# Optimization experiments

Measured on AMD Instinct MI355X. Metric: run time of the kernel, lower is better.

The kernel has to match this reference:

```python
import jax, jax.numpy as jnp
import numpy as np

B = 262144
STATE_DIM = 12
ACTION_DIM = 1
MSG_DIM = 32
MAX_CHILDREN = 2
EPS = 1e-12  # F.normalize default eps


def _l2norm(x):
    n = jnp.sqrt(jnp.sum(x * x, axis=-1, keepdims=True))
    return x / jnp.maximum(n, EPS)


def setup_inputs() -> dict:
    key = jax.random.key(0)
    ks = jax.random.split(key, 16)

    def lin(kw, kb, out_d, in_d):
        lim = 1.0 / np.sqrt(in_d)
        w = jax.random.uniform(kw, (out_d, in_d), jnp.float32, -lim, lim)
        b = jax.random.uniform(kb, (out_d,), jnp.float32, -lim, lim)
        return w, b

    state = jax.random.normal(ks[0], (B, STATE_DIM), jnp.float32)
    action = jax.random.normal(ks[1], (B, ACTION_DIM), jnp.float32)

    # ModelUp (sNet): fc1, fc2, fc3
    up_w1, up_b1 = lin(ks[2], ks[3], 64, STATE_DIM + ACTION_DIM)
    up_w2, up_b2 = lin(ks[4], ks[5], 64, 64 + MSG_DIM * MAX_CHILDREN)
    up_w3, up_b3 = lin(ks[6], ks[7], MSG_DIM, 64)

    # ModelDownAction.model = MLPBase(msg_dim + action_dim + msg_dim, msg_dim)
    dyn_w1, dyn_b1 = lin(ks[8], ks[9], 400, MSG_DIM + ACTION_DIM + MSG_DIM)
    dyn_w2, dyn_b2 = lin(ks[10], ks[11], 300, 400)
    dyn_w3, dyn_b3 = lin(ks[12], ks[13], MSG_DIM, 300)

    return dict(state=state, action=action,
                up_w1=up_w1, up_b1=up_b1, up_w2=up_w2, up_b2=up_b2,
                up_w3=up_w3, up_b3=up_b3,
                dyn_w1=dyn_w1, dyn_b1=dyn_b1, dyn_w2=dyn_w2, dyn_b2=dyn_b2,
                dyn_w3=dyn_w3, dyn_b3=dyn_b3)


def reference(state, action,
              up_w1, up_b1, up_w2, up_b2, up_w3, up_b3,
              dyn_w1, dyn_b1, dyn_w2, dyn_b2, dyn_w3, dyn_b3):
    # num_limbs == 1, parents = [-1], td = bu = True, disable_fold = True
    x = state                              # (B, state_dim)
    u = action                             # (B, 1)

    # ---- bottom_up_transmission(0): ModelUp with all-zero child messages ----
    m_children = jnp.zeros((B, MSG_DIM * MAX_CHILDREN), x.dtype)
    xu = jnp.concatenate([x, u], axis=-1)
    xu = _l2norm(xu @ up_w1.T + up_b1)                       # (B, 64)
    xum = jnp.tanh(jnp.concatenate([xu, m_children], axis=-1))
    xum = jnp.tanh(xum @ up_w2.T + up_b2)                    # (B, 64)
    msg_up = _l2norm(xum @ up_w3.T + up_b3)                  # (B, msg_dim)

    # ---- top_down_transmission(0): ModelDownAction, state := msg_up ----
    # parent_msg = zeros, self_children_idx = 0 -> msg_in = zeros slice
    msg_in = jnp.zeros((B, MSG_DIM), x.dtype)
    xum2 = jnp.concatenate([msg_up, u, msg_in], axis=-1)     # (B, 2*msg_dim+1)
    h = jax.nn.relu(xum2 @ dyn_w1.T + dyn_b1)                # (B, 400)
    h = jax.nn.relu(h @ dyn_w2.T + dyn_b2)                   # (B, 300)
    delta = h @ dyn_w3.T + dyn_b3                            # (B, msg_dim)

    # stack over num_limbs=1 then squeeze -> (B, msg_dim)
    return delta
```

## Files before the change

### kernel.cpp

```cpp
#include <hip/hip_runtime.h>
#include <stdint.h>

typedef short s16x8 __attribute__((ext_vector_type(8)));
typedef float f32x16 __attribute__((ext_vector_type(16)));
typedef unsigned int u32;
typedef unsigned int u32x2 __attribute__((ext_vector_type(2)));

#define NFRAG 336
#define WS_USHORTS (NFRAG*512)
#define PANEL_FRAGS 14
#define PANEL_BYTES (PANEL_FRAGS*1024)
#define LDS_BYTES (3*PANEL_BYTES)

#define MFMA(a,b,c) __builtin_amdgcn_mfma_f32_32x32x16_bf16((a),(b),(c),0,0,0)

__device__ __forceinline__ unsigned short f2bf(float f){
  u32 x = __builtin_bit_cast(u32, f);
  x += 0x7fffu + ((x >> 16) & 1u);
  return (unsigned short)(x >> 16);
}

__device__ __forceinline__ float bfhi(float b){
  return __builtin_bit_cast(float, (u32)f2bf(b) << 16);
}

__device__ __forceinline__ u32 pkbf(float a, float b){
  u32 r;
  asm("v_cvt_pk_bf16_f32 %0, %1, %2" : "=v"(r) : "v"(a), "v"(b));
  return r;
}

__device__ __forceinline__ float fast_tanh(float x){
  float ax = fabsf(x);
  float e = __expf(-2.0f * ax);
  float r = (1.0f - e) * __builtin_amdgcn_rcpf(1.0f + e);
  return x < 0.0f ? -r : r;
}

__device__ __forceinline__ float halfsum(float s){
  return s + __shfl_xor(s, 32);
}

__device__ __forceinline__ void tile2frags(const f32x16 v, s16x8& f0, s16x8& f1){
  u32 w00 = pkbf(v[0],  v[1]),  w01 = pkbf(v[2],  v[3]);
  u32 w10 = pkbf(v[4],  v[5]),  w11 = pkbf(v[6],  v[7]);
  u32 w20 = pkbf(v[8],  v[9]),  w21 = pkbf(v[10], v[11]);
  u32 w30 = pkbf(v[12], v[13]), w31 = pkbf(v[14], v[15]);
  u32x2 p0 = __builtin_amdgcn_permlane32_swap(w00, w10, false, false);
  u32x2 p1 = __builtin_amdgcn_permlane32_swap(w01, w11, false, false);
  u32x2 p2 = __builtin_amdgcn_permlane32_swap(w20, w30, false, false);
  u32x2 p3 = __builtin_amdgcn_permlane32_swap(w21, w31, false, false);
  int4 r0, r1;
  r0.x = (int)p0[0]; r0.y = (int)p1[0]; r0.z = (int)p0[1]; r0.w = (int)p1[1];
  r1.x = (int)p2[0]; r1.y = (int)p3[0]; r1.z = (int)p2[1]; r1.w = (int)p3[1];
  f0 = __builtin_bit_cast(s16x8, r0);
  f1 = __builtin_bit_cast(s16x8, r1);
}

__global__ void wconv_kernel(const float* __restrict__ uw1, const float* __restrict__ ub1,
                             const float* __restrict__ uw2, const float* __restrict__ ub2,
                             const float* __restrict__ uw3, const float* __restrict__ ub3,
                             const float* __restrict__ dw1, const float* __restrict__ db1,
                             const float* __restrict__ dw2, const float* __restrict__ db2,
                             const float* __restrict__ dw3, const float* __restrict__ db3,
                             unsigned short* __restrict__ wp)
{
  int i = blockIdx.x*256 + threadIdx.x;
  if (i >= WS_USHORTS) return;
  int f    = i >> 9;
  int lane = (i >> 3) & 63;
  int j    = i & 7;
  int row  = lane & 31;
  int k8   = (lane >> 5)*8 + j;
  float v = 0.0f;
  if (f < 2){
    int feat = f*32 + row; int k = k8;
    if (k < 13) v = uw1[feat*13 + k];
    else if (k == 13) v = ub1[feat];
    else if (k == 14) v = ub1[feat] - bfhi(ub1[feat]);
  } else if (f < 12){
    int t = f - 2; int kt = t >> 1, nt = t & 1;
    int feat = nt*32 + row; int k = kt*16 + k8;
    if (k < 64) v = uw2[feat*128 + k];
    else if (k == 64) v = ub2[feat];
    else if (k == 65) v = ub2[feat] - bfhi(ub2[feat]);
  } else if (f < 17){
    int kt = f - 12; int feat = row; int k = kt*16 + k8;
    if (k < 64) v = uw3[feat*64 + k];
    else if (k == 64) v = ub3[feat];
    else if (k == 65) v = ub3[feat] - bfhi(ub3[feat]);
  } else if (f < 56){
    int t = f - 17; int nt = t/3, kt = t%3;
    int feat = nt*32 + row; int k = kt*16 + k8;
    if (feat < 400){
      if (k < 33) v = dw1[feat*65 + k];
      else if (k == 33) v = db1[feat];
      else if (k == 34) v = db1[feat] - bfhi(db1[feat]);
    } else if ((feat == 400 || feat == 401) && k == 33) v = 1.0f;
  } else {
    int t = f - 56; int n = t/56; int r = t%56;
    if (r < 52){
      int kf = r >> 1, nt = r & 1;
      int feat = n*64 + nt*32 + row; int k = kf*16 + k8;
      if (feat < 300){
        if (k < 400) v = dw2[feat*400 + k];
        else if (k == 400) v = db2[feat];
        else if (k == 401) v = db2[feat] - bfhi(db2[feat]);
      } else if ((feat == 300 || feat == 301) && k == 400) v = 1.0f;
    } else {
      int kt = n*4 + (r - 52); int feat = row; int k = kt*16 + k8;
      if (k < 300) v = dw3[feat*300 + k];
      else if (k == 300) v = db3[feat];
      else if (k == 301) v = db3[feat] - bfhi(db3[feat]);
    }
  }
  wp[i] = f2bf(v);
}

__device__ __forceinline__ s16x8 fragF(const char* sm, int f, int ln){
  return *(const s16x8*)(sm + ((f/PANEL_FRAGS) % 3)*PANEL_BYTES
                            + (f % PANEL_FRAGS)*1024 + ln*16);
}

__device__ __forceinline__ void stage14(const unsigned short* wp, char* sm, int panel, int tid){
  char* dst = sm + (panel % 3)*PANEL_BYTES;
  const char* src = (const char*)wp + (size_t)panel*PANEL_BYTES;
  #pragma unroll
  for (int j = 0; j < 3; ++j){
    int off = j*4096 + tid*16;
    __builtin_amdgcn_global_load_lds(
      (const __attribute__((address_space(1))) unsigned int*)(src + off),
      (__attribute__((address_space(3))) unsigned int*)(dst + off), 16, 0, 0);
  }
  int off3 = 12288 + (tid & 127)*16;
  __builtin_amdgcn_global_load_lds(
    (const __attribute__((address_space(1))) unsigned int*)(src + off3),
    (__attribute__((address_space(3))) unsigned int*)(dst + off3), 16, 0, 0);
}

#define BND(P) { \
  __syncthreads(); \
  if ((P)+2 <= 23) stage14(wp, sm, (P)+2, tid); \
}

#define TAIL1(aSrc, oA, oB) { \
  _Pragma("unroll") \
  for (int r = 0; r < 16; ++r) aSrc[r] = fmaxf(aSrc[r], 0.f); \
  tile2frags(aSrc, oA, oB); }

#define D1MM(f0_, acc) { \
  __builtin_amdgcn_s_setprio(1); \
  acc = MFMA(fragF(sm, (f0_)+0, ln), mf0, acc); \
  acc = MFMA(fragF(sm, (f0_)+1, ln), mf1, acc); \
  acc = MFMA(fragF(sm, (f0_)+2, ln), mf2, acc); \
  __builtin_amdgcn_s_setprio(0); }

#define D2R(fb, r0, r1, A0, A1) { \
  __builtin_amdgcn_s_setprio(1); \
  _Pragma("unroll") \
  for (int r = (r0); r < (r1); ++r){ \
    s16x8 hb = h1f[r>>1]; \
    if (r & 1) A1 = MFMA(fragF(sm, (fb)+r, ln), hb, A1); \
    else       A0 = MFMA(fragF(sm, (fb)+r, ln), hb, A0); \
  } \
  __builtin_amdgcn_s_setprio(0); }

#define LOADD3W(fb) { \
  d3w0 = fragF(sm, (fb)+52, ln); \
  d3w1 = fragF(sm, (fb)+53, ln); \
  d3w2 = fragF(sm, (fb)+54, ln); \
  d3w3 = fragF(sm, (fb)+55, ln); }

#define TAILD2_RELU(A0, A1) { \
  _Pragma("unroll") \
  for (int r = 0; r < 16; ++r){ \
    A0[r] = fmaxf(A0[r], 0.f); \
    A1[r] = fmaxf(A1[r], 0.f); \
  } }
#define TAILD2_CVT(A0, A1) { \
  tile2frags(A0, cT0, cT1); \
  tile2frags(A1, cT2, cT3); }
#define TAILD2_D3() { \
  __builtin_amdgcn_s_setprio(1); \
  acc3 = MFMA(d3w0, cT0, acc3); \
  acc3 = MFMA(d3w1, cT1, acc3); \
  acc3 = MFMA(d3w2, cT2, acc3); \
  acc3 = MFMA(d3w3, cT3, acc3); \
  __builtin_amdgcn_s_setprio(0); }

#define CHUNKN(fb, P0, C0_, C1_, PR0, PR1) { \
  BND(P0) \
  C0_ = vzero; C1_ = vzero; \
  D2R(fb, 0, 14, C0_, C1_) \
  TAILD2_RELU(PR0, PR1) \
  BND((P0)+1) \
  D2R(fb, 14, 28, C0_, C1_) \
  TAILD2_CVT(PR0, PR1) \
  BND((P0)+2) \
  D2R(fb, 28, 42, C0_, C1_) \
  TAILD2_D3() \
  BND((P0)+3) \
  D2R(fb, 42, 52, C0_, C1_) \
  LOADD3W(fb) \
}

__global__ __launch_bounds__(256, 2) void fused_kernel(
    const float* __restrict__ state, const float* __restrict__ action,
    const unsigned short* __restrict__ wp, float* __restrict__ out)
{
  __shared__ __align__(1024) char sm[LDS_BYTES];

  const int tid = threadIdx.x;
  const int ln  = tid & 63;
  const int wid = tid >> 6;
  const int c   = ln & 31;
  const int h   = ln >> 5;
  const int rowb = blockIdx.x*128 + wid*32;

  const f32x16 vzero = {};

  const float* xr = state + (size_t)(rowb + c)*12;
  float u = action[rowb + c];
  float4 xa, xbr;
  if (h == 0){
    xa  = *(const float4*)xr;
    xbr = *(const float4*)(xr + 4);
  } else {
    xa  = *(const float4*)(xr + 8);
  }

  stage14(wp, sm, 0, tid);
  stage14(wp, sm, 1, tid);
  BND(0)

  float4 xb = (h == 0) ? xbr : float4{u, 1.0f, 1.0f, 0.0f};
  int4 xw;
  xw.x = pkbf(xa.x, xa.y); xw.y = pkbf(xa.z, xa.w);
  xw.z = pkbf(xb.x, xb.y); xw.w = pkbf(xb.z, xb.w);
  s16x8 xfrag = __builtin_bit_cast(s16x8, xw);
  int4 ow = {0,0,0,0}; if (h == 0) ow.x = 0x3F803F80;
  s16x8 onef = __builtin_bit_cast(s16x8, ow);
  int4 mw = {0,0,0,0};
  if (h == 0){ mw.x = pkbf(u, 1.0f); mw.y = 0x3F80; }
  s16x8 mf2 = __builtin_bit_cast(s16x8, mw);

  s16x8 mf0, mf1;
  {
    s16x8 xf0, xf1, xf2, xf3, tf0, tf1, tf2, tf3;
    {
      f32x16 a0 = {}, a1 = {};
      a0 = MFMA(fragF(sm, 0, ln), xfrag, a0);
      a1 = MFMA(fragF(sm, 1, ln), xfrag, a1);
      float s = 0.f;
      #pragma unroll
      for (int r = 0; r < 16; ++r) s += a0[r]*a0[r] + a1[r]*a1[r];
      s = halfsum(s);
      float inv = __builtin_amdgcn_rsqf(fmaxf(s, 1e-24f));
      #pragma unroll
      for (int r = 0; r < 16; ++r){
        a0[r] = fast_tanh(a0[r]*inv);
        a1[r] = fast_tanh(a1[r]*inv);
      }
      tile2frags(a0, xf0, xf1);
      tile2frags(a1, xf2, xf3);
    }
    {
      f32x16 a0 = {}, a1 = {};
      __builtin_amdgcn_s_setprio(1);
      a0 = MFMA(fragF(sm, 2, ln), xf0, a0);  a1 = MFMA(fragF(sm, 3, ln), xf0, a1);
      a0 = MFMA(fragF(sm, 4, ln), xf1, a0);  a1 = MFMA(fragF(sm, 5, ln), xf1, a1);
      a0 = MFMA(fragF(sm, 6, ln), xf2, a0);  a1 = MFMA(fragF(sm, 7, ln), xf2, a1);
      a0 = MFMA(fragF(sm, 8, ln), xf3, a0);  a1 = MFMA(fragF(sm, 9, ln), xf3, a1);
      a0 = MFMA(fragF(sm,10, ln), onef, a0); a1 = MFMA(fragF(sm,11, ln), onef, a1);
      __builtin_amdgcn_s_setprio(0);
      #pragma unroll
      for (int r = 0; r < 16; ++r){
        a0[r] = fast_tanh(a0[r]);
        a1[r] = fast_tanh(a1[r]);
      }
      tile2frags(a0, tf0, tf1);
      tile2frags(a1, tf2, tf3);
    }
    {
      f32x16 m = {};
      __builtin_amdgcn_s_setprio(1);
      m = MFMA(fragF(sm,12, ln), tf0, m);
      m = MFMA(fragF(sm,13, ln), tf1, m);
      __builtin_amdgcn_s_setprio(0);
      BND(1)
      __builtin_amdgcn_s_setprio(1);
      m = MFMA(fragF(sm,14, ln), tf2, m);
      m = MFMA(fragF(sm,15, ln), tf3, m);
      m = MFMA(fragF(sm,16, ln), onef, m);
      __builtin_amdgcn_s_setprio(0);
      float s = 0.f;
      #pragma unroll
      for (int r = 0; r < 16; ++r) s += m[r]*m[r];
      s = halfsum(s);
      float inv = __builtin_amdgcn_rsqf(fmaxf(s, 1e-24f));
      #pragma unroll
      for (int r = 0; r < 16; ++r) m[r] *= inv;
      tile2frags(m, mf0, mf1);
    }
  }

  s16x8 h1f[26];
  f32x16 aX = vzero, aY = vzero;
  D1MM(17, aX)
  D1MM(20, aY)  TAIL1(aX, h1f[0],  h1f[1])
  aX = vzero; D1MM(23, aX)  TAIL1(aY, h1f[2],  h1f[3])
  aY = vzero;
  __builtin_amdgcn_s_setprio(1);
  aY = MFMA(fragF(sm, 26, ln), mf0, aY);
  aY = MFMA(fragF(sm, 27, ln), mf1, aY);
  __builtin_amdgcn_s_setprio(0);
  BND(2)
  __builtin_amdgcn_s_setprio(1);
  aY = MFMA(fragF(sm, 28, ln), mf2, aY);
  __builtin_amdgcn_s_setprio(0);
  TAIL1(aX, h1f[4], h1f[5])
  aX = vzero; D1MM(29, aX)  TAIL1(aY, h1f[6],  h1f[7])
  aY = vzero; D1MM(32, aY)  TAIL1(aX, h1f[8],  h1f[9])
  aX = vzero; D1MM(35, aX)  TAIL1(aY, h1f[10], h1f[11])
  aY = vzero; D1MM(38, aY)  TAIL1(aX, h1f[12], h1f[13])
  aX = vzero;
  __builtin_amdgcn_s_setprio(1);
  aX = MFMA(fragF(sm, 41, ln), mf0, aX);
  __builtin_amdgcn_s_setprio(0);
  BND(3)
  __builtin_amdgcn_s_setprio(1);
  aX = MFMA(fragF(sm, 42, ln), mf1, aX);
  aX = MFMA(fragF(sm, 43, ln), mf2, aX);
  __builtin_amdgcn_s_setprio(0);
  TAIL1(aY, h1f[14], h1f[15])
  aY = vzero; D1MM(44, aY)  TAIL1(aX, h1f[16], h1f[17])
  aX = vzero; D1MM(47, aX)  TAIL1(aY, h1f[18], h1f[19])
  aY = vzero; D1MM(50, aY)  TAIL1(aX, h1f[20], h1f[21])
  aX = vzero; D1MM(53, aX)  TAIL1(aY, h1f[22], h1f[23])

  f32x16 acc3 = vzero;
  f32x16 dA0, dA1, dB0, dB1;
  s16x8 d3w0, d3w1, d3w2, d3w3, cT0, cT1, cT2, cT3;

  {
    BND(4)
    dA0 = vzero; dA1 = vzero;
    D2R(56, 0, 14, dA0, dA1)
    TAIL1(aX, h1f[24], h1f[25])
    BND(5)
    D2R(56, 14, 28, dA0, dA1)
    BND(6)
    D2R(56, 28, 42, dA0, dA1)
    BND(7)
    D2R(56, 42, 52, dA0, dA1)
    LOADD3W(56)
  }
  CHUNKN(112,  8, dB0, dB1, dA0, dA1)
  CHUNKN(168, 12, dA0, dA1, dB0, dB1)
  CHUNKN(224, 16, dB0, dB1, dA0, dA1)
  CHUNKN(280, 20, dA0, dA1, dB0, dB1)
  TAILD2_RELU(dA0, dA1)
  TAILD2_CVT(dA0, dA1)
  TAILD2_D3()

  float* op = out + (size_t)(rowb + c)*32;
  #pragma unroll
  for (int p = 0; p < 4; ++p){
    float4 v4 = {acc3[4*p+0], acc3[4*p+1], acc3[4*p+2], acc3[4*p+3]};
    *(float4*)(op + p*8 + h*4) = v4;
  }
}

extern "C" void kernel_launch(void* const* d_in, const int* in_sizes, int n_in,
                              void* d_out, int out_size, void* d_ws, size_t ws_size,
                              hipStream_t stream)
{
  const float* state  = (const float*)d_in[0];
  const float* action = (const float*)d_in[1];
  const float* up_w1  = (const float*)d_in[2];
  const float* up_b1  = (const float*)d_in[3];
  const float* up_w2  = (const float*)d_in[4];
  const float* up_b2  = (const float*)d_in[5];
  const float* up_w3  = (const float*)d_in[6];
  const float* up_b3  = (const float*)d_in[7];
  const float* dyn_w1 = (const float*)d_in[8];
  const float* dyn_b1 = (const float*)d_in[9];
  const float* dyn_w2 = (const float*)d_in[10];
  const float* dyn_b2 = (const float*)d_in[11];
  const float* dyn_w3 = (const float*)d_in[12];
  const float* dyn_b3 = (const float*)d_in[13];
  unsigned short* wp = (unsigned short*)d_ws;

  hipLaunchKernelGGL(wconv_kernel, dim3((WS_USHORTS + 255)/256), dim3(256), 0, stream,
                     up_w1, up_b1, up_w2, up_b2, up_w3, up_b3,
                     dyn_w1, dyn_b1, dyn_w2, dyn_b2, dyn_w3, dyn_b3, wp);
  hipLaunchKernelGGL(fused_kernel, dim3(262144/128), dim3(256), 0, stream,
                     state, action, wp, (float*)d_out);
}
```

Before: 92.42 us.

## Load odd dyn-layer-2 weight fragments straight from global into registers

Half of the layer-2 weight fragments (the odd ones) are now read directly from global memory into registers a stage ahead, instead of through LDS. The remaining fragments still come through the LDS panels. Barriers are replaced with an explicit partial vmcnt wait plus s_barrier, so the direct global loads can stay in flight across barriers. This aims to halve the LDS read traffic in the dominant layer, at the cost of more VGPRs for prefetched fragments, fragile hand-counted vmcnt values, and redundant global or L2 reads per wave.

```diff
diff --git a/kernel.cpp b/kernel.cpp
--- a/kernel.cpp
+++ b/kernel.cpp
@@ -122,6 +122,10 @@
                             + (f % PANEL_FRAGS)*1024 + ln*16);
 }
 
+__device__ __forceinline__ s16x8 fragG(const unsigned short* wp, int f, int ln){
+  return *(const s16x8*)(wp + (size_t)f*512 + ln*8);
+}
+
 __device__ __forceinline__ void stage14(const unsigned short* wp, char* sm, int panel, int tid){
   char* dst = sm + (panel % 3)*PANEL_BYTES;
   const char* src = (const char*)wp + (size_t)panel*PANEL_BYTES;
@@ -138,9 +142,30 @@
     (__attribute__((address_space(3))) unsigned int*)(dst + off3), 16, 0, 0);
 }
 
-#define BND(P) { \
-  __syncthreads(); \
+#define STR_(x) #x
+#define STR(x) STR_(x)
+#define BNDW(P, W) { \
+  asm volatile("s_waitcnt vmcnt(" STR(W) ") lgkmcnt(0)" ::: "memory"); \
+  __builtin_amdgcn_s_barrier(); \
+  __builtin_amdgcn_sched_barrier(0); \
   if ((P)+2 <= 23) stage14(wp, sm, (P)+2, tid); \
+}
+
+#define ISSUE7(fb, base, B) { \
+  B##0 = fragG(wp, (fb)+(base)+1,  ln); \
+  B##1 = fragG(wp, (fb)+(base)+3,  ln); \
+  B##2 = fragG(wp, (fb)+(base)+5,  ln); \
+  B##3 = fragG(wp, (fb)+(base)+7,  ln); \
+  B##4 = fragG(wp, (fb)+(base)+9,  ln); \
+  B##5 = fragG(wp, (fb)+(base)+11, ln); \
+  B##6 = fragG(wp, (fb)+(base)+13, ln); \
+}
+#define ISSUE5(fb, B) { \
+  B##0 = fragG(wp, (fb)+43, ln); \
+  B##1 = fragG(wp, (fb)+45, ln); \
+  B##2 = fragG(wp, (fb)+47, ln); \
+  B##3 = fragG(wp, (fb)+49, ln); \
+  B##4 = fragG(wp, (fb)+51, ln); \
 }
 
 #define TAIL1(aSrc, oA, oB) { \
@@ -155,14 +180,36 @@
   acc = MFMA(fragF(sm, (f0_)+2, ln), mf2, acc); \
   __builtin_amdgcn_s_setprio(0); }
 
-#define D2R(fb, r0, r1, A0, A1) { \
+#define D2RX14(fb, base, B, A0, A1) { \
   __builtin_amdgcn_s_setprio(1); \
-  _Pragma("unroll") \
-  for (int r = (r0); r < (r1); ++r){ \
-    s16x8 hb = h1f[r>>1]; \
-    if (r & 1) A1 = MFMA(fragF(sm, (fb)+r, ln), hb, A1); \
-    else       A0 = MFMA(fragF(sm, (fb)+r, ln), hb, A0); \
-  } \
+  A0 = MFMA(fragF(sm,(fb)+(base)+0, ln), h1f[((base)+0)>>1],  A0); \
+  A1 = MFMA(B##0,                        h1f[((base)+1)>>1],  A1); \
+  A0 = MFMA(fragF(sm,(fb)+(base)+2, ln), h1f[((base)+2)>>1],  A0); \
+  A1 = MFMA(B##1,                        h1f[((base)+3)>>1],  A1); \
+  A0 = MFMA(fragF(sm,(fb)+(base)+4, ln), h1f[((base)+4)>>1],  A0); \
+  A1 = MFMA(B##2,                        h1f[((base)+5)>>1],  A1); \
+  A0 = MFMA(fragF(sm,(fb)+(base)+6, ln), h1f[((base)+6)>>1],  A0); \
+  A1 = MFMA(B##3,                        h1f[((base)+7)>>1],  A1); \
+  A0 = MFMA(fragF(sm,(fb)+(base)+8, ln), h1f[((base)+8)>>1],  A0); \
+  A1 = MFMA(B##4,                        h1f[((base)+9)>>1],  A1); \
+  A0 = MFMA(fragF(sm,(fb)+(base)+10,ln), h1f[((base)+10)>>1], A0); \
+  A1 = MFMA(B##5,                        h1f[((base)+11)>>1], A1); \
+  A0 = MFMA(fragF(sm,(fb)+(base)+12,ln), h1f[((base)+12)>>1], A0); \
+  A1 = MFMA(B##6,                        h1f[((base)+13)>>1], A1); \
+  __builtin_amdgcn_s_setprio(0); }
+
+#define D2RX10(fb, B, A0, A1) { \
+  __builtin_amdgcn_s_setprio(1); \
+  A0 = MFMA(fragF(sm,(fb)+42, ln), h1f[21], A0); \
+  A1 = MFMA(B##0,                  h1f[21], A1); \
+  A0 = MFMA(fragF(sm,(fb)+44, ln), h1f[22], A0); \
+  A1 = MFMA(B##1,                  h1f[22], A1); \
+  A0 = MFMA(fragF(sm,(fb)+46, ln), h1f[23], A0); \
+  A1 = MFMA(B##2,                  h1f[23], A1); \
+  A0 = MFMA(fragF(sm,(fb)+48, ln), h1f[24], A0); \
+  A1 = MFMA(B##3,                  h1f[24], A1); \
+  A0 = MFMA(fragF(sm,(fb)+50, ln), h1f[25], A0); \
+  A1 = MFMA(B##4,                  h1f[25], A1); \
   __builtin_amdgcn_s_setprio(0); }
 
 #define LOADD3W(fb) { \
@@ -188,19 +235,23 @@
   acc3 = MFMA(d3w3, cT3, acc3); \
   __builtin_amdgcn_s_setprio(0); }
 
-#define CHUNKN(fb, P0, C0_, C1_, PR0, PR1) { \
-  BND(P0) \
+#define CHUNKX(fb, P0, C0_, C1_, PR0, PR1, ISSUE_NEXT, WLAST) { \
+  BNDW(P0, 11) \
+  ISSUE7(fb, 14, gB) \
   C0_ = vzero; C1_ = vzero; \
-  D2R(fb, 0, 14, C0_, C1_) \
+  D2RX14(fb, 0, gA, C0_, C1_) \
   TAILD2_RELU(PR0, PR1) \
-  BND((P0)+1) \
-  D2R(fb, 14, 28, C0_, C1_) \
+  BNDW((P0)+1, 11) \
+  ISSUE7(fb, 28, gA) \
+  D2RX14(fb, 14, gB, C0_, C1_) \
   TAILD2_CVT(PR0, PR1) \
-  BND((P0)+2) \
-  D2R(fb, 28, 42, C0_, C1_) \
+  BNDW((P0)+2, 11) \
+  ISSUE5(fb, gB) \
+  D2RX14(fb, 28, gA, C0_, C1_) \
   TAILD2_D3() \
-  BND((P0)+3) \
-  D2R(fb, 42, 52, C0_, C1_) \
+  BNDW((P0)+3, WLAST) \
+  ISSUE_NEXT \
+  D2RX10(fb, gB, C0_, C1_) \
   LOADD3W(fb) \
 }
 
@@ -218,6 +269,8 @@
   const int rowb = blockIdx.x*128 + wid*32;
 
   const f32x16 vzero = {};
+  s16x8 gA0, gA1, gA2, gA3, gA4, gA5, gA6;
+  s16x8 gB0, gB1, gB2, gB3, gB4, gB5, gB6;
 
   const float* xr = state + (size_t)(rowb + c)*12;
   float u = action[rowb + c];
@@ -231,7 +284,7 @@
 
   stage14(wp, sm, 0, tid);
   stage14(wp, sm, 1, tid);
-  BND(0)
+  BNDW(0, 4)
 
   float4 xb = (h == 0) ? xbr : float4{u, 1.0f, 1.0f, 0.0f};
   int4 xw;
@@ -287,7 +340,7 @@
       m = MFMA(fragF(sm,12, ln), tf0, m);
       m = MFMA(fragF(sm,13, ln), tf1, m);
       __builtin_amdgcn_s_setprio(0);
-      BND(1)
+      BNDW(1, 4)
       __builtin_amdgcn_s_setprio(1);
       m = MFMA(fragF(sm,14, ln), tf2, m);
       m = MFMA(fragF(sm,15, ln), tf3, m);
@@ -314,7 +367,7 @@
   aY = MFMA(fragF(sm, 26, ln), mf0, aY);
   aY = MFMA(fragF(sm, 27, ln), mf1, aY);
   __builtin_amdgcn_s_setprio(0);
-  BND(2)
+  BNDW(2, 4)
   __builtin_amdgcn_s_setprio(1);
   aY = MFMA(fragF(sm, 28, ln), mf2, aY);
   __builtin_amdgcn_s_setprio(0);
@@ -327,7 +380,8 @@
   __builtin_amdgcn_s_setprio(1);
   aX = MFMA(fragF(sm, 41, ln), mf0, aX);
   __builtin_amdgcn_s_setprio(0);
-  BND(3)
+  BNDW(3, 4)
+  ISSUE7(56, 0, gA)
   __builtin_amdgcn_s_setprio(1);
   aX = MFMA(fragF(sm, 42, ln), mf1, aX);
   aX = MFMA(fragF(sm, 43, ln), mf2, aX);
@@ -343,22 +397,26 @@
   s16x8 d3w0, d3w1, d3w2, d3w3, cT0, cT1, cT2, cT3;
 
   {
-    BND(4)
+    BNDW(4, 11)
+    ISSUE7(56, 14, gB)
     dA0 = vzero; dA1 = vzero;
-    D2R(56, 0, 14, dA0, dA1)
+    D2RX14(56, 0, gA, dA0, dA1)
     TAIL1(aX, h1f[24], h1f[25])
-    BND(5)
-    D2R(56, 14, 28, dA0, dA1)
-    BND(6)
-    D2R(56, 28, 42, dA0, dA1)
-    BND(7)
-    D2R(56, 42, 52, dA0, dA1)
+    BNDW(5, 11)
+    ISSUE7(56, 28, gA)
+    D2RX14(56, 14, gB, dA0, dA1)
+    BNDW(6, 11)
+    ISSUE5(56, gB)
+    D2RX14(56, 28, gA, dA0, dA1)
+    BNDW(7, 9)
+    ISSUE7(112, 0, gA)
+    D2RX10(56, gB, dA0, dA1)
     LOADD3W(56)
   }
-  CHUNKN(112,  8, dB0, dB1, dA0, dA1)
-  CHUNKN(168, 12, dA0, dA1, dB0, dB1)
-  CHUNKN(224, 16, dB0, dB1, dA0, dA1)
-  CHUNKN(280, 20, dA0, dA1, dB0, dB1)
+  CHUNKX(112,  8, dB0, dB1, dA0, dA1, ISSUE7(168, 0, gA), 9)
+  CHUNKX(168, 12, dA0, dA1, dB0, dB1, ISSUE7(224, 0, gA), 9)
+  CHUNKX(224, 16, dB0, dB1, dA0, dA1, ISSUE7(280, 0, gA), 9)
+  CHUNKX(280, 20, dA0, dA1, dB0, dB1, , 5)
   TAILD2_RELU(dA0, dA1)
   TAILD2_CVT(dA0, dA1)
   TAILD2_D3()
```

New measurement: 163.9 us. 77.3% more time.

## Shrink LDS weight panels to 8 fragments and raise occupancy to 4 blocks

Applied to the files above, without the earlier changes.

Cuts each triple-buffered LDS weight panel from 14 to 8 fragments, shrinking shared memory per block from 42KB to 24KB. It raises launch bounds to 4 blocks per CU and reschedules every panel boundary barrier across all layers to match the finer panels. The aim is more resident waves to hide latency, at the cost of more barriers and a tighter per-thread register budget. That budget may force spills of the 26 hidden fragments and the accumulators.

```diff
diff --git a/kernel.cpp b/kernel.cpp
--- a/kernel.cpp
+++ b/kernel.cpp
@@ -8,7 +8,7 @@
 
 #define NFRAG 336
 #define WS_USHORTS (NFRAG*512)
-#define PANEL_FRAGS 14
+#define PANEL_FRAGS 8
 #define PANEL_BYTES (PANEL_FRAGS*1024)
 #define LDS_BYTES (3*PANEL_BYTES)
 
@@ -122,25 +122,21 @@
                             + (f % PANEL_FRAGS)*1024 + ln*16);
 }
 
-__device__ __forceinline__ void stage14(const unsigned short* wp, char* sm, int panel, int tid){
+__device__ __forceinline__ void stage8(const unsigned short* wp, char* sm, int panel, int tid){
   char* dst = sm + (panel % 3)*PANEL_BYTES;
   const char* src = (const char*)wp + (size_t)panel*PANEL_BYTES;
   #pragma unroll
-  for (int j = 0; j < 3; ++j){
+  for (int j = 0; j < 2; ++j){
     int off = j*4096 + tid*16;
     __builtin_amdgcn_global_load_lds(
       (const __attribute__((address_space(1))) unsigned int*)(src + off),
       (__attribute__((address_space(3))) unsigned int*)(dst + off), 16, 0, 0);
   }
-  int off3 = 12288 + (tid & 127)*16;
-  __builtin_amdgcn_global_load_lds(
-    (const __attribute__((address_space(1))) unsigned int*)(src + off3),
-    (__attribute__((address_space(3))) unsigned int*)(dst + off3), 16, 0, 0);
 }
 
 #define BND(P) { \
   __syncthreads(); \
-  if ((P)+2 <= 23) stage14(wp, sm, (P)+2, tid); \
+  if ((P)+2 <= 41) stage8(wp, sm, (P)+2, tid); \
 }
 
 #define TAIL1(aSrc, oA, oB) { \
@@ -188,23 +184,29 @@
   acc3 = MFMA(d3w3, cT3, acc3); \
   __builtin_amdgcn_s_setprio(0); }
 
-#define CHUNKN(fb, P0, C0_, C1_, PR0, PR1) { \
+#define CHUNKP(fb, P0, C0_, C1_, PR0, PR1) { \
   BND(P0) \
   C0_ = vzero; C1_ = vzero; \
-  D2R(fb, 0, 14, C0_, C1_) \
+  D2R(fb, 0, 8, C0_, C1_) \
   TAILD2_RELU(PR0, PR1) \
   BND((P0)+1) \
-  D2R(fb, 14, 28, C0_, C1_) \
+  D2R(fb, 8, 16, C0_, C1_) \
   TAILD2_CVT(PR0, PR1) \
   BND((P0)+2) \
-  D2R(fb, 28, 42, C0_, C1_) \
+  D2R(fb, 16, 24, C0_, C1_) \
   TAILD2_D3() \
   BND((P0)+3) \
-  D2R(fb, 42, 52, C0_, C1_) \
+  D2R(fb, 24, 32, C0_, C1_) \
+  BND((P0)+4) \
+  D2R(fb, 32, 40, C0_, C1_) \
+  BND((P0)+5) \
+  D2R(fb, 40, 48, C0_, C1_) \
+  BND((P0)+6) \
+  D2R(fb, 48, 52, C0_, C1_) \
   LOADD3W(fb) \
 }
 
-__global__ __launch_bounds__(256, 2) void fused_kernel(
+__global__ __launch_bounds__(256, 4) void fused_kernel(
     const float* __restrict__ state, const float* __restrict__ action,
     const unsigned short* __restrict__ wp, float* __restrict__ out)
 {
@@ -229,8 +231,8 @@
     xa  = *(const float4*)(xr + 8);
   }
 
-  stage14(wp, sm, 0, tid);
-  stage14(wp, sm, 1, tid);
+  stage8(wp, sm, 0, tid);
+  stage8(wp, sm, 1, tid);
   BND(0)
 
   float4 xb = (h == 0) ? xbr : float4{u, 1.0f, 1.0f, 0.0f};
@@ -270,6 +272,9 @@
       a0 = MFMA(fragF(sm, 2, ln), xf0, a0);  a1 = MFMA(fragF(sm, 3, ln), xf0, a1);
       a0 = MFMA(fragF(sm, 4, ln), xf1, a0);  a1 = MFMA(fragF(sm, 5, ln), xf1, a1);
       a0 = MFMA(fragF(sm, 6, ln), xf2, a0);  a1 = MFMA(fragF(sm, 7, ln), xf2, a1);
+      __builtin_amdgcn_s_setprio(0);
+      BND(1)
+      __builtin_amdgcn_s_setprio(1);
       a0 = MFMA(fragF(sm, 8, ln), xf3, a0);  a1 = MFMA(fragF(sm, 9, ln), xf3, a1);
       a0 = MFMA(fragF(sm,10, ln), onef, a0); a1 = MFMA(fragF(sm,11, ln), onef, a1);
       __builtin_amdgcn_s_setprio(0);
@@ -286,11 +291,11 @@
       __builtin_amdgcn_s_setprio(1);
       m = MFMA(fragF(sm,12, ln), tf0, m);
       m = MFMA(fragF(sm,13, ln), tf1, m);
-      __builtin_amdgcn_s_setprio(0);
-      BND(1)
-      __builtin_amdgcn_s_setprio(1);
       m = MFMA(fragF(sm,14, ln), tf2, m);
       m = MFMA(fragF(sm,15, ln), tf3, m);
+      __builtin_amdgcn_s_setprio(0);
+      BND(2)
+      __builtin_amdgcn_s_setprio(1);
       m = MFMA(fragF(sm,16, ln), onef, m);
       __builtin_amdgcn_s_setprio(0);
       float s = 0.f;
@@ -308,33 +313,43 @@
   f32x16 aX = vzero, aY = vzero;
   D1MM(17, aX)
   D1MM(20, aY)  TAIL1(aX, h1f[0],  h1f[1])
-  aX = vzero; D1MM(23, aX)  TAIL1(aY, h1f[2],  h1f[3])
-  aY = vzero;
-  __builtin_amdgcn_s_setprio(1);
-  aY = MFMA(fragF(sm, 26, ln), mf0, aY);
-  aY = MFMA(fragF(sm, 27, ln), mf1, aY);
-  __builtin_amdgcn_s_setprio(0);
-  BND(2)
-  __builtin_amdgcn_s_setprio(1);
-  aY = MFMA(fragF(sm, 28, ln), mf2, aY);
-  __builtin_amdgcn_s_setprio(0);
-  TAIL1(aX, h1f[4], h1f[5])
+  aX = vzero;
+  __builtin_amdgcn_s_setprio(1);
+  aX = MFMA(fragF(sm, 23, ln), mf0, aX);
+  __builtin_amdgcn_s_setprio(0);
+  BND(3)
+  __builtin_amdgcn_s_setprio(1);
+  aX = MFMA(fragF(sm, 24, ln), mf1, aX);
+  aX = MFMA(fragF(sm, 25, ln), mf2, aX);
+  __builtin_amdgcn_s_setprio(0);
+  TAIL1(aY, h1f[2], h1f[3])
+  aY = vzero; D1MM(26, aY)  TAIL1(aX, h1f[4],  h1f[5])
   aX = vzero; D1MM(29, aX)  TAIL1(aY, h1f[6],  h1f[7])
+  BND(4)
   aY = vzero; D1MM(32, aY)  TAIL1(aX, h1f[8],  h1f[9])
   aX = vzero; D1MM(35, aX)  TAIL1(aY, h1f[10], h1f[11])
-  aY = vzero; D1MM(38, aY)  TAIL1(aX, h1f[12], h1f[13])
+  aY = vzero;
+  __builtin_amdgcn_s_setprio(1);
+  aY = MFMA(fragF(sm, 38, ln), mf0, aY);
+  aY = MFMA(fragF(sm, 39, ln), mf1, aY);
+  __builtin_amdgcn_s_setprio(0);
+  BND(5)
+  __builtin_amdgcn_s_setprio(1);
+  aY = MFMA(fragF(sm, 40, ln), mf2, aY);
+  __builtin_amdgcn_s_setprio(0);
+  TAIL1(aX, h1f[12], h1f[13])
+  aX = vzero; D1MM(41, aX)  TAIL1(aY, h1f[14], h1f[15])
+  aY = vzero; D1MM(44, aY)  TAIL1(aX, h1f[16], h1f[17])
   aX = vzero;
   __builtin_amdgcn_s_setprio(1);
-  aX = MFMA(fragF(sm, 41, ln), mf0, aX);
-  __builtin_amdgcn_s_setprio(0);
-  BND(3)
-  __builtin_amdgcn_s_setprio(1);
-  aX = MFMA(fragF(sm, 42, ln), mf1, aX);
-  aX = MFMA(fragF(sm, 43, ln), mf2, aX);
-  __builtin_amdgcn_s_setprio(0);
-  TAIL1(aY, h1f[14], h1f[15])
-  aY = vzero; D1MM(44, aY)  TAIL1(aX, h1f[16], h1f[17])
-  aX = vzero; D1MM(47, aX)  TAIL1(aY, h1f[18], h1f[19])
+  aX = MFMA(fragF(sm, 47, ln), mf0, aX);
+  __builtin_amdgcn_s_setprio(0);
+  BND(6)
+  __builtin_amdgcn_s_setprio(1);
+  aX = MFMA(fragF(sm, 48, ln), mf1, aX);
+  aX = MFMA(fragF(sm, 49, ln), mf2, aX);
+  __builtin_amdgcn_s_setprio(0);
+  TAIL1(aY, h1f[18], h1f[19])
   aY = vzero; D1MM(50, aY)  TAIL1(aX, h1f[20], h1f[21])
   aX = vzero; D1MM(53, aX)  TAIL1(aY, h1f[22], h1f[23])
 
@@ -343,22 +358,28 @@
   s16x8 d3w0, d3w1, d3w2, d3w3, cT0, cT1, cT2, cT3;
 
   {
-    BND(4)
+    BND(7)
     dA0 = vzero; dA1 = vzero;
-    D2R(56, 0, 14, dA0, dA1)
+    D2R(56, 0, 8, dA0, dA1)
     TAIL1(aX, h1f[24], h1f[25])
-    BND(5)
-    D2R(56, 14, 28, dA0, dA1)
-    BND(6)
-    D2R(56, 28, 42, dA0, dA1)
-    BND(7)
-    D2R(56, 42, 52, dA0, dA1)
+    BND(8)
+    D2R(56, 8, 16, dA0, dA1)
+    BND(9)
+    D2R(56, 16, 24, dA0, dA1)
+    BND(10)
+    D2R(56, 24, 32, dA0, dA1)
+    BND(11)
+    D2R(56, 32, 40, dA0, dA1)
+    BND(12)
+    D2R(56, 40, 48, dA0, dA1)
+    BND(13)
+    D2R(56, 48, 52, dA0, dA1)
     LOADD3W(56)
   }
-  CHUNKN(112,  8, dB0, dB1, dA0, dA1)
-  CHUNKN(168, 12, dA0, dA1, dB0, dB1)
-  CHUNKN(224, 16, dB0, dB1, dA0, dA1)
-  CHUNKN(280, 20, dA0, dA1, dB0, dB1)
+  CHUNKP(112, 14, dB0, dB1, dA0, dA1)
+  CHUNKP(168, 21, dA0, dA1, dB0, dB1)
+  CHUNKP(224, 28, dB0, dB1, dA0, dA1)
+  CHUNKP(280, 35, dA0, dA1, dB0, dB1)
   TAILD2_RELU(dA0, dA1)
   TAILD2_CVT(dA0, dA1)
   TAILD2_D3()
```

New measurement: 201.1 us. 118% more time.
